# Optimization experiments

Hardware: AMD Instinct MI355X
Metric: run time of the kernel (lower is better)

Reference implementation:

```python
import jax, jax.numpy as jnp
import numpy as np

N_NODES = 100000
N_EDGES = 1600000
IN_C, HID_C, OUT_C = 128, 64, 32


def setup_inputs() -> dict:
    key = jax.random.key(0)
    k1, k2, k3, k4 = jax.random.split(key, 4)
    x = jax.random.normal(k1, (N_NODES, IN_C), dtype=jnp.float32)
    edge_index = jax.random.randint(k2, (2, N_EDGES), 0, N_NODES, dtype=jnp.int64)
    # glorot-style init for GCN linear weights
    W1 = jax.random.normal(k3, (IN_C, HID_C), dtype=jnp.float32) * (2.0 / (IN_C + HID_C)) ** 0.5
    b1 = jnp.zeros((HID_C,), dtype=jnp.float32)
    W2 = jax.random.normal(k4, (HID_C, OUT_C), dtype=jnp.float32) * (2.0 / (HID_C + OUT_C)) ** 0.5
    b2 = jnp.zeros((OUT_C,), dtype=jnp.float32)
    return {"x": x, "edge_index": edge_index, "W1": W1, "b1": b1, "W2": W2, "b2": b2}


def _gcn_conv(h, row, col, norm, n, b):
    # gather transformed source features, scale by symmetric norm, scatter-add to targets
    msg = h[row] * norm[:, None]            # [E+N, C]
    return jax.ops.segment_sum(msg, col, num_segments=n) + b


def reference(x, edge_index, W1, b1, W2, b2):
    n = x.shape[0]
    loops = jnp.arange(n, dtype=edge_index.dtype)
    row = jnp.concatenate([edge_index[0], loops])   # sources (with self-loops)
    col = jnp.concatenate([edge_index[1], loops])   # targets
    deg = jax.ops.segment_sum(jnp.ones_like(col, dtype=x.dtype), col, num_segments=n)
    dinv = jnp.where(deg > 0, jax.lax.rsqrt(deg), 0.0)
    norm = dinv[row] * dinv[col]                    # D^{-1/2} A_hat D^{-1/2}
    h = jax.nn.relu(_gcn_conv(x @ W1, row, col, norm, n, b1))
    out = _gcn_conv(h @ W2, row, col, norm, n, b2)
    return out
```

## Files before the change

kernel.cpp:

```cpp
#include <hip/hip_runtime.h>

#define IN_C 128
#define HID_C 64
#define OUT_C 32
#define NBLK 512
#define NBUCK 512
#define CAP 5120

typedef unsigned int uint;
typedef unsigned short ushort;
typedef __attribute__((ext_vector_type(8))) short bf16x8;
typedef __attribute__((ext_vector_type(4))) float f32x4;

__device__ __forceinline__ uint bf16pair(float a, float b) {
  uint ua = __float_as_uint(a), ub = __float_as_uint(b);
  ua = (ua + 0x7FFFu + ((ua >> 16) & 1u)) >> 16;
  ub = (ub + 0x7FFFu + ((ub >> 16) & 1u)) >> 16;
  return ua | (ub << 16);
}

__device__ __forceinline__ uint bf16one(float a) {
  uint u = __float_as_uint(a);
  return (u + 0x7FFFu + ((u >> 16) & 1u)) >> 16;
}

__device__ __forceinline__ void acc8(float* acc, uint4 q) {
  acc[0] += __uint_as_float(q.x << 16);
  acc[1] += __uint_as_float(q.x & 0xFFFF0000u);
  acc[2] += __uint_as_float(q.y << 16);
  acc[3] += __uint_as_float(q.y & 0xFFFF0000u);
  acc[4] += __uint_as_float(q.z << 16);
  acc[5] += __uint_as_float(q.z & 0xFFFF0000u);
  acc[6] += __uint_as_float(q.w << 16);
  acc[7] += __uint_as_float(q.w & 0xFFFF0000u);
}


__global__ void __launch_bounds__(256) scatter_reserve_kernel(
    const int* __restrict__ row, const int* __restrict__ col,
    int* __restrict__ gcur, int* __restrict__ ebuf, int e, int epb) {
  __shared__ int hist[NBUCK];
  __shared__ int cur[NBUCK];
  int t = threadIdx.x, b = blockIdx.x;
  for (int i = t; i < NBUCK; i += 256) hist[i] = 0;
  __syncthreads();
  int s = b * epb, en = min(e, s + epb);
  for (int i = s + t; i < en; i += 256) atomicAdd(&hist[col[i] >> 8], 1);
  __syncthreads();
  for (int i = t; i < NBUCK; i += 256) {
    int h = hist[i];
    int base = h ? atomicAdd(&gcur[i], h) : 0;
    cur[i] = CAP * i + base;
  }
  __syncthreads();
  for (int i = s + t; i < en; i += 256) {
    int c = col[i], r = row[i];
    int bk = c >> 8;
    int p = atomicAdd(&cur[bk], 1);
    if (p < CAP * bk + CAP) ebuf[p] = r | ((c & 255) << 17);
  }
}

__global__ void __launch_bounds__(256) csr_kernel(const int* __restrict__ ebuf,
                                                  const int* __restrict__ gcur,
                                                  int* __restrict__ offS, int* __restrict__ offE,
                                                  int* __restrict__ srt, float* __restrict__ dinv,
                                                  int n) {
  __shared__ int cnt[256];
  __shared__ int base[256];
  int t = threadIdx.x, b = blockIdx.x;
  int es = b * CAP;
  int ec = min(gcur[b], CAP);
  cnt[t] = 0;
  __syncthreads();
  for (int i = t; i < ec; i += 256) atomicAdd(&cnt[(ebuf[es + i] >> 17) & 255], 1);
  __syncthreads();
  int v = cnt[t];
  base[t] = v;
  __syncthreads();
  for (int d = 1; d < 256; d <<= 1) {
    int a = (t >= d) ? base[t - d] : 0;
    __syncthreads();
    base[t] += a;
    __syncthreads();
  }
  int gstart = es + base[t] - v;
  int node = b * 256 + t;
  if (node < n) {
    offS[node] = gstart;
    offE[node] = gstart + v;
    dinv[node] = rsqrtf((float)(v + 1));
  }
  base[t] = gstart;
  __syncthreads();
  for (int i = t; i < ec; i += 256) {
    int pv = ebuf[es + i];
    int pos = atomicAdd(&base[(pv >> 17) & 255], 1);
    srt[pos] = pv & 0x1FFFF;
  }
}


__global__ void __launch_bounds__(256) prep_w1t_kernel(const float* __restrict__ W1,
                                                       ushort* __restrict__ w1t_hi,
                                                       ushort* __restrict__ w1t_lo) {
  int t = threadIdx.x;
  for (int i = t; i < HID_C * IN_C; i += 256) {
    int c = i >> 7, k = i & 127;
    float v = W1[k * HID_C + c];
    uint h = bf16one(v);
    float lo = v - __uint_as_float(h << 16);
    w1t_hi[i] = (ushort)h;
    w1t_lo[i] = (ushort)bf16one(lo);
  }
}

#define APAD 136
__global__ void __launch_bounds__(256) gemm1_mfma_kernel(
    const float* __restrict__ x, const ushort* __restrict__ w1t_hi,
    const ushort* __restrict__ w1t_lo, const float* __restrict__ dinv,
    ushort* __restrict__ xw1b, int n) {
  __shared__ ushort xs_hi[64 * APAD];
  __shared__ ushort xs_lo[64 * APAD];
  __shared__ float dinv_s[64];
  int t = threadIdx.x;
  int row0 = blockIdx.x * 64;
  if (t < 64) {
    int rr = row0 + t;
    dinv_s[t] = rr < n ? dinv[rr] : 0.f;
  }
  for (int task = t; task < 64 * 16; task += 256) {
    int r = task >> 4, kc = task & 15;
    int grow = row0 + r;
    uint4 hq = {0u, 0u, 0u, 0u}, lq = {0u, 0u, 0u, 0u};
    if (grow < n) {
      const float* xp = x + (size_t)grow * IN_C + kc * 8;
      float4 v0 = *(const float4*)xp;
      float4 v1 = *(const float4*)(xp + 4);
      float vv[8] = {v0.x, v0.y, v0.z, v0.w, v1.x, v1.y, v1.z, v1.w};
      uint hu[8];
      float lf[8];
#pragma unroll
      for (int i = 0; i < 8; ++i) {
        hu[i] = bf16one(vv[i]);
        lf[i] = vv[i] - __uint_as_float(hu[i] << 16);
      }
      hq = make_uint4(hu[0] | (hu[1] << 16), hu[2] | (hu[3] << 16),
                      hu[4] | (hu[5] << 16), hu[6] | (hu[7] << 16));
      lq = make_uint4(bf16pair(lf[0], lf[1]), bf16pair(lf[2], lf[3]),
                      bf16pair(lf[4], lf[5]), bf16pair(lf[6], lf[7]));
    }
    *(uint4*)(xs_hi + r * APAD + kc * 8) = hq;
    *(uint4*)(xs_lo + r * APAD + kc * 8) = lq;
  }
  __syncthreads();
  int wv = t >> 6, lane = t & 63, m = lane & 15, q = lane >> 4;
  f32x4 acc[4];
#pragma unroll
  for (int ct = 0; ct < 4; ++ct) acc[ct] = (f32x4){0.f, 0.f, 0.f, 0.f};
  const ushort* ah_p = xs_hi + (wv * 16 + m) * APAD + q * 8;
  const ushort* al_p = xs_lo + (wv * 16 + m) * APAD + q * 8;
#pragma unroll
  for (int kb = 0; kb < 4; ++kb) {
    bf16x8 ah = *(const bf16x8*)(ah_p + kb * 32);
    bf16x8 al = *(const bf16x8*)(al_p + kb * 32);
#pragma unroll
    for (int ct = 0; ct < 4; ++ct) {
      const ushort* bp = w1t_hi + (ct * 16 + m) * IN_C + kb * 32 + q * 8;
      bf16x8 bh = *(const bf16x8*)bp;
      bf16x8 bl = *(const bf16x8*)(bp + (size_t)(w1t_lo - w1t_hi));
      acc[ct] = __builtin_amdgcn_mfma_f32_16x16x32_bf16(ah, bh, acc[ct], 0, 0, 0);
      acc[ct] = __builtin_amdgcn_mfma_f32_16x16x32_bf16(al, bh, acc[ct], 0, 0, 0);
      acc[ct] = __builtin_amdgcn_mfma_f32_16x16x32_bf16(ah, bl, acc[ct], 0, 0, 0);
    }
  }
#pragma unroll
  for (int ct = 0; ct < 4; ++ct) {
#pragma unroll
    for (int rg = 0; rg < 4; ++rg) {
      int lr = wv * 16 + q * 4 + rg;
      int grow = row0 + lr;
      if (grow < n)
        xw1b[(size_t)grow * HID_C + ct * 16 + m] = (ushort)bf16one(acc[ct][rg] * dinv_s[lr]);
    }
  }
}

__global__ void __launch_bounds__(256) gather1_gemm2_kernel(
    const int* __restrict__ offS, const int* __restrict__ offE, const int* __restrict__ srt,
    const float* __restrict__ dinv, const ushort* __restrict__ xw1b,
    const float* __restrict__ b1, const float* __restrict__ W2,
    ushort* __restrict__ hw2b, int n) {
  __shared__ float w2s[HID_C * OUT_C];
  __shared__ float hs[32][HID_C];
  int t = threadIdx.x;
  for (int i = t; i < HID_C * OUT_C; i += 256) w2s[i] = W2[i];
  int g = t >> 3, fl = t & 7;
  int c = blockIdx.x * 32 + g;
  if (c < n) {
    int js = offS[c], je = offE[c];
    float acc[8] = {0.f, 0.f, 0.f, 0.f, 0.f, 0.f, 0.f, 0.f};
    float acc2[8] = {0.f, 0.f, 0.f, 0.f, 0.f, 0.f, 0.f, 0.f};
    int j = js;
    for (; j + 3 < je; j += 4) {
      int r0 = __builtin_nontemporal_load(srt + j);
      int r1 = __builtin_nontemporal_load(srt + j + 1);
      int r2 = __builtin_nontemporal_load(srt + j + 2);
      int r3 = __builtin_nontemporal_load(srt + j + 3);
      uint4 q0 = ((const uint4*)(xw1b + (size_t)r0 * HID_C))[fl];
      uint4 q1 = ((const uint4*)(xw1b + (size_t)r1 * HID_C))[fl];
      uint4 q2 = ((const uint4*)(xw1b + (size_t)r2 * HID_C))[fl];
      uint4 q3 = ((const uint4*)(xw1b + (size_t)r3 * HID_C))[fl];
      acc8(acc, q0); acc8(acc2, q1); acc8(acc, q2); acc8(acc2, q3);
    }
    for (; j < je; ++j) {
      int r = __builtin_nontemporal_load(srt + j);
      acc8(acc, ((const uint4*)(xw1b + (size_t)r * HID_C))[fl]);
    }
    acc8(acc, ((const uint4*)(xw1b + (size_t)c * HID_C))[fl]);
    float dv = dinv[c];
    const float4* b1v = (const float4*)b1;
    float4 blo = b1v[fl * 2], bhi = b1v[fl * 2 + 1];
    float h0 = (acc[0] + acc2[0]) * dv + blo.x;
    float h1 = (acc[1] + acc2[1]) * dv + blo.y;
    float h2 = (acc[2] + acc2[2]) * dv + blo.z;
    float h3 = (acc[3] + acc2[3]) * dv + blo.w;
    float h4 = (acc[4] + acc2[4]) * dv + bhi.x;
    float h5 = (acc[5] + acc2[5]) * dv + bhi.y;
    float h6 = (acc[6] + acc2[6]) * dv + bhi.z;
    float h7 = (acc[7] + acc2[7]) * dv + bhi.w;
    float4 lo = {h0 > 0.f ? h0 : 0.f, h1 > 0.f ? h1 : 0.f,
                 h2 > 0.f ? h2 : 0.f, h3 > 0.f ? h3 : 0.f};
    float4 hi = {h4 > 0.f ? h4 : 0.f, h5 > 0.f ? h5 : 0.f,
                 h6 > 0.f ? h6 : 0.f, h7 > 0.f ? h7 : 0.f};
    ((float4*)hs[g])[fl * 2] = lo;
    ((float4*)hs[g])[fl * 2 + 1] = hi;
  }
  __syncthreads();
  for (int task = t; task < 32 * (OUT_C / 2); task += 256) {
    int nl = task >> 4, pr = task & 15;
    int c2 = blockIdx.x * 32 + nl;
    if (c2 < n) {
      float s0 = 0.f, s1 = 0.f;
      const float* hr = hs[nl];
#pragma unroll
      for (int k = 0; k < HID_C; ++k) {
        float hv = hr[k];
        s0 += hv * w2s[k * OUT_C + pr * 2];
        s1 += hv * w2s[k * OUT_C + pr * 2 + 1];
      }
      float dv2 = dinv[c2];
      ((uint*)(hw2b + (size_t)c2 * OUT_C))[pr] = bf16pair(s0 * dv2, s1 * dv2);
    }
  }
}

__global__ void __launch_bounds__(256) gather2_kernel(
    const int* __restrict__ offS, const int* __restrict__ offE, const int* __restrict__ srt,
    const float* __restrict__ dinv, const ushort* __restrict__ hw2b,
    const float* __restrict__ b2, float* __restrict__ out, int n) {
  int t = threadIdx.x;
  int g = t >> 2, fl = t & 3;
  int c = blockIdx.x * 64 + g;
  if (c >= n) return;
  int js = offS[c], je = offE[c];
  float acc[8] = {0.f, 0.f, 0.f, 0.f, 0.f, 0.f, 0.f, 0.f};
  float acc2[8] = {0.f, 0.f, 0.f, 0.f, 0.f, 0.f, 0.f, 0.f};
  int j = js;
  for (; j + 3 < je; j += 4) {
    int r0 = __builtin_nontemporal_load(srt + j);
    int r1 = __builtin_nontemporal_load(srt + j + 1);
    int r2 = __builtin_nontemporal_load(srt + j + 2);
    int r3 = __builtin_nontemporal_load(srt + j + 3);
    uint4 q0 = ((const uint4*)(hw2b + (size_t)r0 * OUT_C))[fl];
    uint4 q1 = ((const uint4*)(hw2b + (size_t)r1 * OUT_C))[fl];
    uint4 q2 = ((const uint4*)(hw2b + (size_t)r2 * OUT_C))[fl];
    uint4 q3 = ((const uint4*)(hw2b + (size_t)r3 * OUT_C))[fl];
    acc8(acc, q0); acc8(acc2, q1); acc8(acc, q2); acc8(acc2, q3);
  }
  for (; j < je; ++j) {
    int r = __builtin_nontemporal_load(srt + j);
    acc8(acc, ((const uint4*)(hw2b + (size_t)r * OUT_C))[fl]);
  }
  acc8(acc, ((const uint4*)(hw2b + (size_t)c * OUT_C))[fl]);
  float dv = dinv[c];
  const float4* b2v = (const float4*)b2;
  float4 blo = b2v[fl * 2], bhi = b2v[fl * 2 + 1];
  float4 olo = {(acc[0] + acc2[0]) * dv + blo.x, (acc[1] + acc2[1]) * dv + blo.y,
                (acc[2] + acc2[2]) * dv + blo.z, (acc[3] + acc2[3]) * dv + blo.w};
  float4 ohi = {(acc[4] + acc2[4]) * dv + bhi.x, (acc[5] + acc2[5]) * dv + bhi.y,
                (acc[6] + acc2[6]) * dv + bhi.z, (acc[7] + acc2[7]) * dv + bhi.w};
  ((float4*)(out + (size_t)c * OUT_C))[fl * 2] = olo;
  ((float4*)(out + (size_t)c * OUT_C))[fl * 2 + 1] = ohi;
}

extern "C" void kernel_launch(void* const* d_in, const int* in_sizes, int n_in,
                              void* d_out, int out_size, void* d_ws, size_t ws_size,
                              hipStream_t stream) {
  const float* x  = (const float*)d_in[0];
  const int*   ei = (const int*)d_in[1];
  const float* W1 = (const float*)d_in[2];
  const float* b1 = (const float*)d_in[3];
  const float* W2 = (const float*)d_in[4];
  const float* b2 = (const float*)d_in[5];
  float* out = (float*)d_out;

  int n = in_sizes[0] / IN_C;
  int e = in_sizes[1] / 2;
  const int* row = ei;
  const int* col = ei + e;

  float* dinv = (float*)d_ws;
  int*   offS = (int*)(dinv + n);
  int*   offE = offS + n;
  int*   gcur = offE + n;
  int*   srt  = gcur + NBUCK;
  ushort* xw1b = (ushort*)(srt + (size_t)NBUCK * CAP);
  int*   ebuf = (int*)xw1b;
  ushort* hw2b = xw1b + (size_t)n * HID_C;
  ushort* w1t_hi = hw2b + (size_t)n * OUT_C;
  ushort* w1t_lo = w1t_hi + HID_C * IN_C;

  int epb = (e + NBLK - 1) / NBLK;
  int nbuckets = (n + 255) / 256;

  hipMemsetAsync(gcur, 0, NBUCK * sizeof(int), stream);
  hipLaunchKernelGGL(scatter_reserve_kernel, dim3(NBLK), dim3(256), 0, stream,
                     row, col, gcur, ebuf, e, epb);
  hipLaunchKernelGGL(csr_kernel, dim3(nbuckets), dim3(256), 0, stream,
                     ebuf, gcur, offS, offE, srt, dinv, n);
  hipLaunchKernelGGL(prep_w1t_kernel, dim3(1), dim3(256), 0, stream, W1, w1t_hi, w1t_lo);
  hipLaunchKernelGGL(gemm1_mfma_kernel, dim3((n + 63) / 64), dim3(256), 0, stream,
                     x, w1t_hi, w1t_lo, dinv, xw1b, n);
  hipLaunchKernelGGL(gather1_gemm2_kernel, dim3((n + 31) / 32), dim3(256), 0, stream,
                     offS, offE, srt, dinv, xw1b, b1, W2, hw2b, n);
  hipLaunchKernelGGL(gather2_kernel, dim3((n + 63) / 64), dim3(256), 0, stream,
                     offS, offE, srt, dinv, hw2b, b2, out, n);
}
```

Baseline: 249.0 us.

## Split gather features into column planes and move GEMM2 to MFMA kernel

```diff
diff --git a/kernel.cpp b/kernel.cpp
--- a/kernel.cpp
+++ b/kernel.cpp
@@ -22,17 +22,6 @@
 __device__ __forceinline__ uint bf16one(float a) {
   uint u = __float_as_uint(a);
   return (u + 0x7FFFu + ((u >> 16) & 1u)) >> 16;
-}
-
-__device__ __forceinline__ void acc8(float* acc, uint4 q) {
-  acc[0] += __uint_as_float(q.x << 16);
-  acc[1] += __uint_as_float(q.x & 0xFFFF0000u);
-  acc[2] += __uint_as_float(q.y << 16);
-  acc[3] += __uint_as_float(q.y & 0xFFFF0000u);
-  acc[4] += __uint_as_float(q.z << 16);
-  acc[5] += __uint_as_float(q.z & 0xFFFF0000u);
-  acc[6] += __uint_as_float(q.w << 16);
-  acc[7] += __uint_as_float(q.w & 0xFFFF0000u);
 }
 
 
@@ -101,9 +90,12 @@
 }
 
 
-__global__ void __launch_bounds__(256) prep_w1t_kernel(const float* __restrict__ W1,
-                                                       ushort* __restrict__ w1t_hi,
-                                                       ushort* __restrict__ w1t_lo) {
+__global__ void __launch_bounds__(256) prep_w_kernel(const float* __restrict__ W1,
+                                                     const float* __restrict__ W2,
+                                                     ushort* __restrict__ w1t_hi,
+                                                     ushort* __restrict__ w1t_lo,
+                                                     ushort* __restrict__ w2t_hi,
+                                                     ushort* __restrict__ w2t_lo) {
   int t = threadIdx.x;
   for (int i = t; i < HID_C * IN_C; i += 256) {
     int c = i >> 7, k = i & 127;
@@ -113,13 +105,21 @@
     w1t_hi[i] = (ushort)h;
     w1t_lo[i] = (ushort)bf16one(lo);
   }
+  for (int i = t; i < OUT_C * HID_C; i += 256) {
+    int c = i >> 6, k = i & 63;
+    float v = W2[k * OUT_C + c];
+    uint h = bf16one(v);
+    float lo = v - __uint_as_float(h << 16);
+    w2t_hi[i] = (ushort)h;
+    w2t_lo[i] = (ushort)bf16one(lo);
+  }
 }
 
 #define APAD 136
 __global__ void __launch_bounds__(256) gemm1_mfma_kernel(
     const float* __restrict__ x, const ushort* __restrict__ w1t_hi,
     const ushort* __restrict__ w1t_lo, const float* __restrict__ dinv,
-    ushort* __restrict__ xw1b, int n) {
+    ushort* __restrict__ xw1q, int n, int planeN) {
   __shared__ ushort xs_hi[64 * APAD];
   __shared__ ushort xs_lo[64 * APAD];
   __shared__ float dinv_s[64];
@@ -181,117 +181,121 @@
       int lr = wv * 16 + q * 4 + rg;
       int grow = row0 + lr;
       if (grow < n)
-        xw1b[(size_t)grow * HID_C + ct * 16 + m] = (ushort)bf16one(acc[ct][rg] * dinv_s[lr]);
-    }
-  }
-}
-
-__global__ void __launch_bounds__(256) gather1_gemm2_kernel(
+        xw1q[(size_t)ct * planeN + (size_t)grow * 16 + m] =
+            (ushort)bf16one(acc[ct][rg] * dinv_s[lr]);
+    }
+  }
+}
+
+
+__global__ void __launch_bounds__(256) gather1_plane_kernel(
     const int* __restrict__ offS, const int* __restrict__ offE, const int* __restrict__ srt,
-    const float* __restrict__ dinv, const ushort* __restrict__ xw1b,
-    const float* __restrict__ b1, const float* __restrict__ W2,
-    ushort* __restrict__ hw2b, int n) {
-  __shared__ float w2s[HID_C * OUT_C];
-  __shared__ float hs[32][HID_C];
+    const float* __restrict__ dinv, const ushort* __restrict__ xw1q,
+    const float* __restrict__ b1, ushort* __restrict__ hb, int n, int planeN) {
+  int t = threadIdx.x, bid = blockIdx.x;
+  int pq = bid & 3, chunk = bid >> 2;
+  int g = t >> 3, fl = t & 7, lane = t & 63;
+  int c = chunk * 32 + g;
+  if (c >= n) return;
+  const uint* tbl = (const uint*)(xw1q + (size_t)pq * planeN);
+  int js = offS[c], je = offE[c];
+  float aL[4] = {0.f, 0.f, 0.f, 0.f}, aH[4] = {0.f, 0.f, 0.f, 0.f};
+  for (int j = js; j < je; j += 8) {
+    int idx = __builtin_nontemporal_load(srt + min(j + fl, je - 1));
+#pragma unroll
+    for (int k = 0; k < 8; ++k) {
+      int r = __shfl(idx, (lane & 56) | k, 64);
+      if (j + k < je) {
+        uint w = tbl[(size_t)r * 8 + fl];
+        aL[k & 3] += __uint_as_float(w << 16);
+        aH[k & 3] += __uint_as_float(w & 0xFFFF0000u);
+      }
+    }
+  }
+  uint ws = tbl[(size_t)c * 8 + fl];
+  aL[0] += __uint_as_float(ws << 16);
+  aH[0] += __uint_as_float(ws & 0xFFFF0000u);
+  float dv = dinv[c];
+  float2 bb = ((const float2*)b1)[pq * 8 + fl];
+  float h0 = ((aL[0] + aL[1]) + (aL[2] + aL[3])) * dv + bb.x;
+  float h1 = ((aH[0] + aH[1]) + (aH[2] + aH[3])) * dv + bb.y;
+  h0 = h0 > 0.f ? h0 : 0.f;
+  h1 = h1 > 0.f ? h1 : 0.f;
+  ((uint*)hb)[(size_t)c * 32 + pq * 8 + fl] = bf16pair(h0, h1);
+}
+
+__global__ void __launch_bounds__(256) gemm2_mfma_kernel(
+    const ushort* __restrict__ hb, const ushort* __restrict__ w2t_hi,
+    const ushort* __restrict__ w2t_lo, const float* __restrict__ dinv,
+    ushort* __restrict__ hw2h, int n, int planeN) {
   int t = threadIdx.x;
-  for (int i = t; i < HID_C * OUT_C; i += 256) w2s[i] = W2[i];
-  int g = t >> 3, fl = t & 7;
-  int c = blockIdx.x * 32 + g;
-  if (c < n) {
-    int js = offS[c], je = offE[c];
-    float acc[8] = {0.f, 0.f, 0.f, 0.f, 0.f, 0.f, 0.f, 0.f};
-    float acc2[8] = {0.f, 0.f, 0.f, 0.f, 0.f, 0.f, 0.f, 0.f};
-    int j = js;
-    for (; j + 3 < je; j += 4) {
-      int r0 = __builtin_nontemporal_load(srt + j);
-      int r1 = __builtin_nontemporal_load(srt + j + 1);
-      int r2 = __builtin_nontemporal_load(srt + j + 2);
-      int r3 = __builtin_nontemporal_load(srt + j + 3);
-      uint4 q0 = ((const uint4*)(xw1b + (size_t)r0 * HID_C))[fl];
-      uint4 q1 = ((const uint4*)(xw1b + (size_t)r1 * HID_C))[fl];
-      uint4 q2 = ((const uint4*)(xw1b + (size_t)r2 * HID_C))[fl];
-      uint4 q3 = ((const uint4*)(xw1b + (size_t)r3 * HID_C))[fl];
-      acc8(acc, q0); acc8(acc2, q1); acc8(acc, q2); acc8(acc2, q3);
-    }
-    for (; j < je; ++j) {
-      int r = __builtin_nontemporal_load(srt + j);
-      acc8(acc, ((const uint4*)(xw1b + (size_t)r * HID_C))[fl]);
-    }
-    acc8(acc, ((const uint4*)(xw1b + (size_t)c * HID_C))[fl]);
-    float dv = dinv[c];
-    const float4* b1v = (const float4*)b1;
-    float4 blo = b1v[fl * 2], bhi = b1v[fl * 2 + 1];
-    float h0 = (acc[0] + acc2[0]) * dv + blo.x;
-    float h1 = (acc[1] + acc2[1]) * dv + blo.y;
-    float h2 = (acc[2] + acc2[2]) * dv + blo.z;
-    float h3 = (acc[3] + acc2[3]) * dv + blo.w;
-    float h4 = (acc[4] + acc2[4]) * dv + bhi.x;
-    float h5 = (acc[5] + acc2[5]) * dv + bhi.y;
-    float h6 = (acc[6] + acc2[6]) * dv + bhi.z;
-    float h7 = (acc[7] + acc2[7]) * dv + bhi.w;
-    float4 lo = {h0 > 0.f ? h0 : 0.f, h1 > 0.f ? h1 : 0.f,
-                 h2 > 0.f ? h2 : 0.f, h3 > 0.f ? h3 : 0.f};
-    float4 hi = {h4 > 0.f ? h4 : 0.f, h5 > 0.f ? h5 : 0.f,
-                 h6 > 0.f ? h6 : 0.f, h7 > 0.f ? h7 : 0.f};
-    ((float4*)hs[g])[fl * 2] = lo;
-    ((float4*)hs[g])[fl * 2 + 1] = hi;
-  }
-  __syncthreads();
-  for (int task = t; task < 32 * (OUT_C / 2); task += 256) {
-    int nl = task >> 4, pr = task & 15;
-    int c2 = blockIdx.x * 32 + nl;
-    if (c2 < n) {
-      float s0 = 0.f, s1 = 0.f;
-      const float* hr = hs[nl];
-#pragma unroll
-      for (int k = 0; k < HID_C; ++k) {
-        float hv = hr[k];
-        s0 += hv * w2s[k * OUT_C + pr * 2];
-        s1 += hv * w2s[k * OUT_C + pr * 2 + 1];
+  int wv = t >> 6, lane = t & 63, m = lane & 15, q = lane >> 4;
+  int row0 = blockIdx.x * 64 + wv * 16;
+  int arow = min(row0 + m, n - 1);
+  const ushort* ap = hb + (size_t)arow * HID_C + q * 8;
+  bf16x8 a0 = *(const bf16x8*)ap;
+  bf16x8 a1 = *(const bf16x8*)(ap + 32);
+  f32x4 acc[2];
+  acc[0] = (f32x4){0.f, 0.f, 0.f, 0.f};
+  acc[1] = (f32x4){0.f, 0.f, 0.f, 0.f};
+#pragma unroll
+  for (int ct = 0; ct < 2; ++ct) {
+    const ushort* bp = w2t_hi + (ct * 16 + m) * HID_C + q * 8;
+    const ushort* blp = w2t_lo + (ct * 16 + m) * HID_C + q * 8;
+    bf16x8 bh0 = *(const bf16x8*)bp;
+    bf16x8 bh1 = *(const bf16x8*)(bp + 32);
+    bf16x8 bl0 = *(const bf16x8*)blp;
+    bf16x8 bl1 = *(const bf16x8*)(blp + 32);
+    acc[ct] = __builtin_amdgcn_mfma_f32_16x16x32_bf16(a0, bh0, acc[ct], 0, 0, 0);
+    acc[ct] = __builtin_amdgcn_mfma_f32_16x16x32_bf16(a1, bh1, acc[ct], 0, 0, 0);
+    acc[ct] = __builtin_amdgcn_mfma_f32_16x16x32_bf16(a0, bl0, acc[ct], 0, 0, 0);
+    acc[ct] = __builtin_amdgcn_mfma_f32_16x16x32_bf16(a1, bl1, acc[ct], 0, 0, 0);
+  }
+#pragma unroll
+  for (int ct = 0; ct < 2; ++ct) {
+#pragma unroll
+    for (int rg = 0; rg < 4; ++rg) {
+      int node = row0 + q * 4 + rg;
+      if (node < n)
+        hw2h[(size_t)ct * planeN + (size_t)node * 16 + m] =
+            (ushort)bf16one(acc[ct][rg] * dinv[node]);
+    }
+  }
+}
+
+__global__ void __launch_bounds__(256) gather2_plane_kernel(
+    const int* __restrict__ offS, const int* __restrict__ offE, const int* __restrict__ srt,
+    const float* __restrict__ dinv, const ushort* __restrict__ hw2h,
+    const float* __restrict__ b2, float* __restrict__ out, int n, int planeN) {
+  int t = threadIdx.x, bid = blockIdx.x;
+  int ph = bid & 1, chunk = bid >> 1;
+  int g = t >> 3, fl = t & 7, lane = t & 63;
+  int c = chunk * 32 + g;
+  if (c >= n) return;
+  const uint* tbl = (const uint*)(hw2h + (size_t)ph * planeN);
+  int js = offS[c], je = offE[c];
+  float aL[4] = {0.f, 0.f, 0.f, 0.f}, aH[4] = {0.f, 0.f, 0.f, 0.f};
+  for (int j = js; j < je; j += 8) {
+    int idx = __builtin_nontemporal_load(srt + min(j + fl, je - 1));
+#pragma unroll
+    for (int k = 0; k < 8; ++k) {
+      int r = __shfl(idx, (lane & 56) | k, 64);
+      if (j + k < je) {
+        uint w = tbl[(size_t)r * 8 + fl];
+        aL[k & 3] += __uint_as_float(w << 16);
+        aH[k & 3] += __uint_as_float(w & 0xFFFF0000u);
       }
-      float dv2 = dinv[c2];
-      ((uint*)(hw2b + (size_t)c2 * OUT_C))[pr] = bf16pair(s0 * dv2, s1 * dv2);
-    }
-  }
-}
-
-__global__ void __launch_bounds__(256) gather2_kernel(
-    const int* __restrict__ offS, const int* __restrict__ offE, const int* __restrict__ srt,
-    const float* __restrict__ dinv, const ushort* __restrict__ hw2b,
-    const float* __restrict__ b2, float* __restrict__ out, int n) {
-  int t = threadIdx.x;
-  int g = t >> 2, fl = t & 3;
-  int c = blockIdx.x * 64 + g;
-  if (c >= n) return;
-  int js = offS[c], je = offE[c];
-  float acc[8] = {0.f, 0.f, 0.f, 0.f, 0.f, 0.f, 0.f, 0.f};
-  float acc2[8] = {0.f, 0.f, 0.f, 0.f, 0.f, 0.f, 0.f, 0.f};
-  int j = js;
-  for (; j + 3 < je; j += 4) {
-    int r0 = __builtin_nontemporal_load(srt + j);
-    int r1 = __builtin_nontemporal_load(srt + j + 1);
-    int r2 = __builtin_nontemporal_load(srt + j + 2);
-    int r3 = __builtin_nontemporal_load(srt + j + 3);
-    uint4 q0 = ((const uint4*)(hw2b + (size_t)r0 * OUT_C))[fl];
-    uint4 q1 = ((const uint4*)(hw2b + (size_t)r1 * OUT_C))[fl];
-    uint4 q2 = ((const uint4*)(hw2b + (size_t)r2 * OUT_C))[fl];
-    uint4 q3 = ((const uint4*)(hw2b + (size_t)r3 * OUT_C))[fl];
-    acc8(acc, q0); acc8(acc2, q1); acc8(acc, q2); acc8(acc2, q3);
-  }
-  for (; j < je; ++j) {
-    int r = __builtin_nontemporal_load(srt + j);
-    acc8(acc, ((const uint4*)(hw2b + (size_t)r * OUT_C))[fl]);
-  }
-  acc8(acc, ((const uint4*)(hw2b + (size_t)c * OUT_C))[fl]);
+    }
+  }
+  uint ws = tbl[(size_t)c * 8 + fl];
+  aL[0] += __uint_as_float(ws << 16);
+  aH[0] += __uint_as_float(ws & 0xFFFF0000u);
   float dv = dinv[c];
-  const float4* b2v = (const float4*)b2;
-  float4 blo = b2v[fl * 2], bhi = b2v[fl * 2 + 1];
-  float4 olo = {(acc[0] + acc2[0]) * dv + blo.x, (acc[1] + acc2[1]) * dv + blo.y,
-                (acc[2] + acc2[2]) * dv + blo.z, (acc[3] + acc2[3]) * dv + blo.w};
-  float4 ohi = {(acc[4] + acc2[4]) * dv + bhi.x, (acc[5] + acc2[5]) * dv + bhi.y,
-                (acc[6] + acc2[6]) * dv + bhi.z, (acc[7] + acc2[7]) * dv + bhi.w};
-  ((float4*)(out + (size_t)c * OUT_C))[fl * 2] = olo;
-  ((float4*)(out + (size_t)c * OUT_C))[fl * 2 + 1] = ohi;
+  float2 bb = ((const float2*)b2)[ph * 8 + fl];
+  float2 o2;
+  o2.x = ((aL[0] + aL[1]) + (aL[2] + aL[3])) * dv + bb.x;
+  o2.y = ((aH[0] + aH[1]) + (aH[2] + aH[3])) * dv + bb.y;
+  ((float2*)out)[(size_t)c * 16 + ph * 8 + fl] = o2;
 }
 
 extern "C" void kernel_launch(void* const* d_in, const int* in_sizes, int n_in,
@@ -309,31 +313,39 @@
   int e = in_sizes[1] / 2;
   const int* row = ei;
   const int* col = ei + e;
+  int planeN = n * 16;
 
   float* dinv = (float*)d_ws;
   int*   offS = (int*)(dinv + n);
   int*   offE = offS + n;
   int*   gcur = offE + n;
   int*   srt  = gcur + NBUCK;
-  ushort* xw1b = (ushort*)(srt + (size_t)NBUCK * CAP);
-  int*   ebuf = (int*)xw1b;
-  ushort* hw2b = xw1b + (size_t)n * HID_C;
-  ushort* w1t_hi = hw2b + (size_t)n * OUT_C;
+  ushort* xw1q = (ushort*)(srt + (size_t)NBUCK * CAP);
+  int*   ebuf = (int*)xw1q;
+  ushort* hb   = xw1q + (size_t)n * HID_C;
+  ushort* hw2h = hb + (size_t)n * HID_C;
+  ushort* w1t_hi = hw2h + (size_t)n * OUT_C;
   ushort* w1t_lo = w1t_hi + HID_C * IN_C;
+  ushort* w2t_hi = w1t_lo + HID_C * IN_C;
+  ushort* w2t_lo = w2t_hi + OUT_C * HID_C;
 
   int epb = (e + NBLK - 1) / NBLK;
   int nbuckets = (n + 255) / 256;
+  int chunks = (n + 31) / 32;
 
   hipMemsetAsync(gcur, 0, NBUCK * sizeof(int), stream);
   hipLaunchKernelGGL(scatter_reserve_kernel, dim3(NBLK), dim3(256), 0, stream,
                      row, col, gcur, ebuf, e, epb);
   hipLaunchKernelGGL(csr_kernel, dim3(nbuckets), dim3(256), 0, stream,
                      ebuf, gcur, offS, offE, srt, dinv, n);
-  hipLaunchKernelGGL(prep_w1t_kernel, dim3(1), dim3(256), 0, stream, W1, w1t_hi, w1t_lo);
+  hipLaunchKernelGGL(prep_w_kernel, dim3(1), dim3(256), 0, stream,
+                     W1, W2, w1t_hi, w1t_lo, w2t_hi, w2t_lo);
   hipLaunchKernelGGL(gemm1_mfma_kernel, dim3((n + 63) / 64), dim3(256), 0, stream,
-                     x, w1t_hi, w1t_lo, dinv, xw1b, n);
-  hipLaunchKernelGGL(gather1_gemm2_kernel, dim3((n + 31) / 32), dim3(256), 0, stream,
-                     offS, offE, srt, dinv, xw1b, b1, W2, hw2b, n);
-  hipLaunchKernelGGL(gather2_kernel, dim3((n + 63) / 64), dim3(256), 0, stream,
-                     offS, offE, srt, dinv, hw2b, b2, out, n);
-}
+                     x, w1t_hi, w1t_lo, dinv, xw1q, n, planeN);
+  hipLaunchKernelGGL(gather1_plane_kernel, dim3(chunks * 4), dim3(256), 0, stream,
+                     offS, offE, srt, dinv, xw1q, b1, hb, n, planeN);
+  hipLaunchKernelGGL(gemm2_mfma_kernel, dim3((n + 63) / 64), dim3(256), 0, stream,
+                     hb, w2t_hi, w2t_lo, dinv, hw2h, n, planeN);
+  hipLaunchKernelGGL(gather2_plane_kernel, dim3(chunks * 2), dim3(256), 0, stream,
+                     offS, offE, srt, dinv, hw2h, b2, out, n, planeN);
+}
```

After: 315.6 us. 1.27x slower.
